# Kernel optimization log

Hardware: AMD Instinct MI355X
Metric: run time of the kernel (lower is better)

Reference implementation:

```python
import jax, jax.numpy as jnp
import numpy as np

# Llama config (TinyLlama-scale)
L, H, KVH, D = 2, 32, 8, 64      # layers, q heads, kv heads, head_dim
DM, FF, V = 2048, 8192, 32000    # d_model, intermediate, vocab
B, S = 1, 1024                   # batch, seq_len
EPS, THETA = 1e-5, 10000.0


def setup_inputs() -> dict:
    key = jax.random.key(0)
    ks = jax.random.split(key, 10)
    w = lambda k, shape: jax.random.normal(k, shape, jnp.float32) * 0.02
    return {
        "input_ids": jax.random.randint(ks[0], (B, S), 0, V, dtype=jnp.int32),
        "embed": w(ks[1], (V, DM)),
        "wq": w(ks[2], (L, DM, H * D)),
        "wk": w(ks[3], (L, DM, KVH * D)),
        "wv": w(ks[4], (L, DM, KVH * D)),
        "wo": w(ks[5], (L, H * D, DM)),
        "wgate": w(ks[6], (L, DM, FF)),
        "wup": w(ks[7], (L, DM, FF)),
        "wdown": w(ks[8], (L, FF, DM)),
        "ln1": jnp.ones((L, DM), jnp.float32),
        "ln2": jnp.ones((L, DM), jnp.float32),
    }


def _rms(h, g):
    return h * jax.lax.rsqrt(jnp.mean(h * h, axis=-1, keepdims=True) + EPS) * g


def _rotate_half(t):
    t1, t2 = jnp.split(t, 2, axis=-1)
    return jnp.concatenate([-t2, t1], axis=-1)


def reference(input_ids, embed, wq, wk, wv, wo, wgate, wup, wdown, ln1, ln2):
    x = embed[input_ids]                                  # (B,S,DM)
    # rotary embeddings (HF llama style)
    inv_freq = 1.0 / (THETA ** (jnp.arange(0, D, 2, dtype=jnp.float32) / D))
    freqs = jnp.arange(S, dtype=jnp.float32)[:, None] * inv_freq[None, :]
    emb = jnp.concatenate([freqs, freqs], axis=-1)        # (S,D)
    cos = jnp.cos(emb)[None, None]                        # (1,1,S,D)
    sin = jnp.sin(emb)[None, None]
    # eager causal additive mask (1,1,S,S)
    mask = jnp.triu(jnp.full((1, 1, S, S), jnp.finfo(jnp.float32).min, jnp.float32), k=1)
    scale = 1.0 / np.sqrt(D).astype(np.float32)
    for l in range(L):
        # self-attention block
        h = _rms(x, ln1[l])
        q = (h @ wq[l]).reshape(B, S, H, D).transpose(0, 2, 1, 3)     # (B,H,S,D)
        k = (h @ wk[l]).reshape(B, S, KVH, D).transpose(0, 2, 1, 3)   # (B,KVH,S,D)
        v = (h @ wv[l]).reshape(B, S, KVH, D).transpose(0, 2, 1, 3)
        q = q * cos + _rotate_half(q) * sin
        k = k * cos + _rotate_half(k) * sin
        k = jnp.repeat(k, H // KVH, axis=1)                           # GQA expand
        v = jnp.repeat(v, H // KVH, axis=1)
        scores = jnp.einsum('bhqd,bhkd->bhqk', q, k) * scale + mask   # eager path
        probs = jax.nn.softmax(scores, axis=-1)
        attn = jnp.einsum('bhqk,bhkd->bhqd', probs, v)
        attn = attn.transpose(0, 2, 1, 3).reshape(B, S, H * D)
        x = x + attn @ wo[l]
        # SwiGLU MLP block
        h = _rms(x, ln2[l])
        x = x + (jax.nn.silu(h @ wgate[l]) * (h @ wup[l])) @ wdown[l]
    return x
```

## Files before the change

kernel.cpp:

```cpp
#include <hip/hip_runtime.h>
#include <hip/hip_bf16.h>
#include <math.h>

#define NL 2
#define NH 32
#define NKVH 8
#define HD 64
#define DM 2048
#define FF 8192
#define SEQ 1024
#define QKVW 3072
#define RMS_EPS 1e-5f

typedef short s8v __attribute__((ext_vector_type(8)));
typedef short s4v __attribute__((ext_vector_type(4)));
typedef float f32x4 __attribute__((ext_vector_type(4)));
typedef __hip_bfloat16 bf16;

__global__ __launch_bounds__(256) void embed_kernel(const int* __restrict__ ids,
                                                    const float* __restrict__ emb,
                                                    float* __restrict__ x) {
    int s = blockIdx.x;
    int row = ids[s];
    const float4* src = (const float4*)(emb + (size_t)row * DM);
    float4* dst = (float4*)(x + (size_t)s * DM);
    #pragma unroll
    for (int i = 0; i < 2; ++i)
        dst[threadIdx.x + i * 256] = src[threadIdx.x + i * 256];
}

__global__ __launch_bounds__(256) void rms_kernel(const float* __restrict__ x,
                                                  const float* __restrict__ g,
                                                  bf16* __restrict__ out) {
    int s = blockIdx.x;
    const float4* row = (const float4*)(x + (size_t)s * DM);
    float4 v0 = row[threadIdx.x * 2];
    float4 v1 = row[threadIdx.x * 2 + 1];
    float ss = v0.x*v0.x + v0.y*v0.y + v0.z*v0.z + v0.w*v0.w
             + v1.x*v1.x + v1.y*v1.y + v1.z*v1.z + v1.w*v1.w;
    #pragma unroll
    for (int o = 32; o > 0; o >>= 1) ss += __shfl_down(ss, o, 64);
    __shared__ float red[4];
    if ((threadIdx.x & 63) == 0) red[threadIdx.x >> 6] = ss;
    __syncthreads();
    float total = red[0] + red[1] + red[2] + red[3];
    float inv = 1.0f / sqrtf(total / (float)DM + RMS_EPS);
    const float4* g4 = (const float4*)g;
    float4 ga = g4[threadIdx.x * 2], gb = g4[threadIdx.x * 2 + 1];
    union { bf16 h[8]; s8v v; } u;
    u.h[0] = __float2bfloat16(v0.x * inv * ga.x);
    u.h[1] = __float2bfloat16(v0.y * inv * ga.y);
    u.h[2] = __float2bfloat16(v0.z * inv * ga.z);
    u.h[3] = __float2bfloat16(v0.w * inv * ga.w);
    u.h[4] = __float2bfloat16(v1.x * inv * gb.x);
    u.h[5] = __float2bfloat16(v1.y * inv * gb.y);
    u.h[6] = __float2bfloat16(v1.z * inv * gb.z);
    u.h[7] = __float2bfloat16(v1.w * inv * gb.w);
    *(s8v*)(out + (size_t)s * DM + threadIdx.x * 8) = u.v;
}

template<bool OUTBF>
__global__ __launch_bounds__(256) void gemm_f32w_kernel(const bf16* __restrict__ A, int Ka,
                                                        const float* __restrict__ Wa, int Na,
                                                        const float* __restrict__ Wb, int Nb,
                                                        const float* __restrict__ Wc,
                                                        float* __restrict__ C,
                                                        bf16* __restrict__ Cb,
                                                        int M, int N, int Kchunk) {
    __shared__ bf16 As[2][128 * 64];
    __shared__ bf16 Bs[2][128 * 64];
    const int t = threadIdx.x, lane = t & 63;
    const int w = t >> 6;
    const int m0 = blockIdx.y * 128, n0 = blockIdx.x * 128;
    const size_t koff = (size_t)blockIdx.z * Kchunk;

    const int nl = t & 127;
    const int kob = t >> 7;
    const int ng = n0 + nl;
    const float* wp; int wstr;
    if (ng < Na)           { wp = Wa + ng;             wstr = Na; }
    else if (ng < Na + Nb) { wp = Wb + (ng - Na);      wstr = Nb; }
    else                   { wp = Wc + (ng - Na - Nb); wstr = N - Na - Nb; }
    wp += koff * (size_t)wstr;

    const int ako = t & 7, am = t >> 3;
    const bf16* apt = A + (size_t)(m0 + am) * Ka + koff + ako * 8;

    const int wm = (w >> 1) * 64, wn = (w & 1) * 64;
    const int fr = lane & 15, sl = lane >> 4;

    f32x4 acc[4][4];
    f32x4 z = {0.f, 0.f, 0.f, 0.f};
    #pragma unroll
    for (int i = 0; i < 4; ++i)
        #pragma unroll
        for (int j = 0; j < 4; ++j) acc[i][j] = z;

    float rb[4][8];
    s8v ra[4];

    auto LOADR = [&](int tile) {
        const int k0 = tile * 64;
        #pragma unroll
        for (int u = 0; u < 4; ++u) {
            const float* p = wp + (size_t)(k0 + (kob + 2 * u) * 8) * wstr;
            #pragma unroll
            for (int j = 0; j < 8; ++j) rb[u][j] = p[(size_t)j * wstr];
            ra[u] = *(const s8v*)(apt + (size_t)(32 * u) * Ka + k0);
        }
    };
    auto WRITE = [&](bf16* AsB, bf16* BsB) {
        #pragma unroll
        for (int u = 0; u < 4; ++u) {
            union { bf16 h[8]; s8v v; } cv;
            #pragma unroll
            for (int j = 0; j < 8; ++j) cv.h[j] = __float2bfloat16(rb[u][j]);
            int ko = kob + 2 * u;
            *(s8v*)((char*)BsB + nl * 128 + ((ko * 16) ^ ((nl & 7) << 4))) = cv.v;
            int m = am + 32 * u;
            *(s8v*)((char*)AsB + m * 128 + ((ako * 16) ^ ((m & 7) << 4))) = ra[u];
        }
    };
    auto COMPUTE = [&](const bf16* AsB, const bf16* BsB) {
        #pragma unroll
        for (int kk = 0; kk < 2; ++kk) {
            const int kb = kk * 64 + sl * 16;
            s8v af[4], bfv[4];
            #pragma unroll
            for (int i = 0; i < 4; ++i) {
                int m = wm + i * 16 + fr;
                af[i] = *(const s8v*)((const char*)AsB + m * 128 + (kb ^ ((m & 7) << 4)));
            }
            #pragma unroll
            for (int j = 0; j < 4; ++j) {
                int n = wn + j * 16 + fr;
                bfv[j] = *(const s8v*)((const char*)BsB + n * 128 + (kb ^ ((n & 7) << 4)));
            }
            #pragma unroll
            for (int i = 0; i < 4; ++i)
                #pragma unroll
                for (int j = 0; j < 4; ++j)
                    acc[i][j] = __builtin_amdgcn_mfma_f32_16x16x32_bf16(af[i], bfv[j], acc[i][j], 0, 0, 0);
        }
    };

    const int nt = Kchunk / 64;
    LOADR(0);
    WRITE(&As[0][0], &Bs[0][0]);
    __syncthreads();
    for (int tt = 0; tt < nt; ++tt) {
        const int cur = tt & 1;
        if (tt + 1 < nt) LOADR(tt + 1);
        COMPUTE(&As[cur][0], &Bs[cur][0]);
        if (tt + 1 < nt) {
            __syncthreads();
            WRITE(&As[cur ^ 1][0], &Bs[cur ^ 1][0]);
            __syncthreads();
        }
    }

    float* Cz = C + (size_t)blockIdx.z * M * N;
    #pragma unroll
    for (int i = 0; i < 4; ++i) {
        #pragma unroll
        for (int j = 0; j < 4; ++j) {
            #pragma unroll
            for (int q = 0; q < 4; ++q) {
                int row = m0 + wm + i * 16 + sl * 4 + q;
                int col = n0 + wn + j * 16 + fr;
                float vv = acc[i][j][q];
                if constexpr (OUTBF) Cb[(size_t)row * N + col] = __float2bfloat16(vv);
                else                 Cz[(size_t)row * N + col] = vv;
            }
        }
    }
}

__global__ __launch_bounds__(256) void reduce4_kernel(float* __restrict__ x,
                                                      const float* __restrict__ p) {
    const int n4 = SEQ * DM / 4;
    int i = blockIdx.x * 256 + threadIdx.x;
    if (i >= n4) return;
    float4 a = ((const float4*)x)[i];
    #pragma unroll
    for (int c = 0; c < 4; ++c) {
        float4 v = ((const float4*)p)[i + c * n4];
        a.x += v.x; a.y += v.y; a.z += v.z; a.w += v.w;
    }
    ((float4*)x)[i] = a;
}

__global__ __launch_bounds__(256) void rope_qk_kernel(const float* __restrict__ qkv,
                                                      bf16* __restrict__ Qh,
                                                      bf16* __restrict__ Kh) {
    int idx = blockIdx.x * 256 + threadIdx.x;
    int i = idx & 31;
    int hh = (idx >> 5) % (NH + NKVH);
    int s = idx / (32 * (NH + NKVH));
    bool isq = hh < NH;
    int col = isq ? hh * HD + i : DM + (hh - NH) * HD + i;
    float a = qkv[(size_t)s * QKVW + col];
    float b = qkv[(size_t)s * QKVW + col + 32];
    float inv = exp2f(-(float)i * 0.41524101186092029f);
    float ang = (float)s * inv;
    float c = cosf(ang), sn = sinf(ang);
    float ra = a * c - b * sn;
    float rb = b * c + a * sn;
    if (isq) {
        bf16* p = Qh + ((size_t)hh * SEQ + s) * HD + i;
        p[0]  = __float2bfloat16(ra);
        p[32] = __float2bfloat16(rb);
    } else {
        bf16* p = Kh + ((size_t)(hh - NH) * SEQ + s) * HD + i;
        p[0]  = __float2bfloat16(ra);
        p[32] = __float2bfloat16(rb);
    }
}

__global__ __launch_bounds__(256) void vtrans_kernel(const float* __restrict__ qkv,
                                                     bf16* __restrict__ Vt) {
    __shared__ float tile[64][65];
    const int s0 = blockIdx.x * 64;
    const int kvh = blockIdx.y;
    const int tx = threadIdx.x & 63, ty = threadIdx.x >> 6;
    #pragma unroll
    for (int i = 0; i < 16; ++i)
        tile[i * 4 + ty][tx] = qkv[(size_t)(s0 + i * 4 + ty) * QKVW + DM + 512 + kvh * HD + tx];
    __syncthreads();
    #pragma unroll
    for (int i = 0; i < 16; ++i) {
        int d = i * 4 + ty;
        Vt[((size_t)kvh * HD + d) * SEQ + s0 + tx] = __float2bfloat16(tile[tx][d]);
    }
}

__global__ __launch_bounds__(256) void attn_mfma_kernel(const bf16* __restrict__ Qh,
                                                        const bf16* __restrict__ Kh,
                                                        const bf16* __restrict__ Vt,
                                                        bf16* __restrict__ o) {
    __shared__ char lds[32768];
    char* Qs = lds;
    char* Ks = lds + 8192;
    char* Vs = lds + 16384;
    char* Ps = lds + 24576;
    const int t = threadIdx.x, lane = t & 63, w = t >> 6;
    const int g = lane >> 4, lo = lane & 15;
    const int h = blockIdx.y, kvh = h >> 2;
    const int qbase = blockIdx.x * 64;
    const int strip = w * 16;
    const bf16* qsrc = Qh + ((size_t)h * SEQ + qbase) * HD;
    const bf16* ksrc = Kh + (size_t)kvh * SEQ * HD;
    const bf16* vsrc = Vt + (size_t)kvh * HD * SEQ;

    #pragma unroll
    for (int c = t; c < 512; c += 256) {
        int row = c >> 3, col = c & 7;
        *(s8v*)(Qs + row * 128 + ((col * 16) ^ ((row & 7) << 4))) =
            *(const s8v*)(qsrc + row * HD + col * 8);
    }

    f32x4 oacc[4];
    f32x4 z = {0.f, 0.f, 0.f, 0.f};
    #pragma unroll
    for (int dj = 0; dj < 4; ++dj) oacc[dj] = z;
    float m0[4], lsum[4];
    #pragma unroll
    for (int r = 0; r < 4; ++r) { m0[r] = -INFINITY; lsum[r] = 0.f; }

    const int qt = blockIdx.x;
    for (int kt = 0; kt <= qt; ++kt) {
        __syncthreads();
        const bf16* kq = ksrc + (size_t)(kt * 64) * HD;
        const bf16* vq = vsrc + kt * 64;
        #pragma unroll
        for (int c = t; c < 512; c += 256) {
            int row = c >> 3, col = c & 7;
            int swz = (col * 16) ^ ((row & 7) << 4);
            *(s8v*)(Ks + row * 128 + swz) = *(const s8v*)(kq + row * HD + col * 8);
            *(s8v*)(Vs + row * 128 + swz) = *(const s8v*)(vq + (size_t)row * SEQ + col * 8);
        }
        __syncthreads();

        s8v qa0 = *(const s8v*)(Qs + (strip + lo) * 128 + ((g * 16) ^ ((lo & 7) << 4)));
        s8v qa1 = *(const s8v*)(Qs + (strip + lo) * 128 + ((64 + g * 16) ^ ((lo & 7) << 4)));
        f32x4 sacc[4];
        #pragma unroll
        for (int j = 0; j < 4; ++j) {
            s8v kb0 = *(const s8v*)(Ks + (j * 16 + lo) * 128 + ((g * 16) ^ ((lo & 7) << 4)));
            s8v kb1 = *(const s8v*)(Ks + (j * 16 + lo) * 128 + ((64 + g * 16) ^ ((lo & 7) << 4)));
            f32x4 sv = __builtin_amdgcn_mfma_f32_16x16x32_bf16(qa0, kb0, z, 0, 0, 0);
            sacc[j] = __builtin_amdgcn_mfma_f32_16x16x32_bf16(qa1, kb1, sv, 0, 0, 0);
        }
        #pragma unroll
        for (int j = 0; j < 4; ++j) {
            int kgl = kt * 64 + j * 16 + lo;
            #pragma unroll
            for (int r = 0; r < 4; ++r) {
                int qgl = qbase + strip + g * 4 + r;
                float sv = sacc[j][r] * 0.125f;
                sacc[j][r] = (kgl <= qgl) ? sv : -INFINITY;
            }
        }
        float rmax[4], resc[4];
        #pragma unroll
        for (int r = 0; r < 4; ++r) {
            float mx = fmaxf(fmaxf(sacc[0][r], sacc[1][r]), fmaxf(sacc[2][r], sacc[3][r]));
            mx = fmaxf(mx, __shfl_xor(mx, 1, 64));
            mx = fmaxf(mx, __shfl_xor(mx, 2, 64));
            mx = fmaxf(mx, __shfl_xor(mx, 4, 64));
            mx = fmaxf(mx, __shfl_xor(mx, 8, 64));
            float mn = fmaxf(m0[r], mx);
            resc[r] = expf(m0[r] - mn);
            m0[r] = mn;
            rmax[r] = mn;
        }
        #pragma unroll
        for (int j = 0; j < 4; ++j)
            #pragma unroll
            for (int r = 0; r < 4; ++r)
                sacc[j][r] = expf(sacc[j][r] - rmax[r]);
        #pragma unroll
        for (int r = 0; r < 4; ++r) {
            float ps = sacc[0][r] + sacc[1][r] + sacc[2][r] + sacc[3][r];
            lsum[r] = lsum[r] * resc[r] + ps;
        }
        #pragma unroll
        for (int dj = 0; dj < 4; ++dj)
            #pragma unroll
            for (int r = 0; r < 4; ++r)
                oacc[dj][r] *= resc[r];
        #pragma unroll
        for (int j = 0; j < 4; ++j) {
            #pragma unroll
            for (int r = 0; r < 4; ++r) {
                int prow = strip + g * 4 + r;
                int pcol = j * 16 + lo;
                *(bf16*)(Ps + prow * 128 + ((pcol * 2) ^ ((prow & 7) << 4))) =
                    __float2bfloat16(sacc[j][r]);
            }
        }
        s8v pa0 = *(const s8v*)(Ps + (strip + lo) * 128 + ((g * 16) ^ ((lo & 7) << 4)));
        s8v pa1 = *(const s8v*)(Ps + (strip + lo) * 128 + ((64 + g * 16) ^ ((lo & 7) << 4)));
        #pragma unroll
        for (int dj = 0; dj < 4; ++dj) {
            s8v vb0 = *(const s8v*)(Vs + (dj * 16 + lo) * 128 + ((g * 16) ^ ((lo & 7) << 4)));
            s8v vb1 = *(const s8v*)(Vs + (dj * 16 + lo) * 128 + ((64 + g * 16) ^ ((lo & 7) << 4)));
            oacc[dj] = __builtin_amdgcn_mfma_f32_16x16x32_bf16(pa0, vb0, oacc[dj], 0, 0, 0);
            oacc[dj] = __builtin_amdgcn_mfma_f32_16x16x32_bf16(pa1, vb1, oacc[dj], 0, 0, 0);
        }
    }
    float invl[4];
    #pragma unroll
    for (int r = 0; r < 4; ++r) {
        float l = lsum[r];
        l += __shfl_xor(l, 1, 64);
        l += __shfl_xor(l, 2, 64);
        l += __shfl_xor(l, 4, 64);
        l += __shfl_xor(l, 8, 64);
        invl[r] = 1.f / l;
    }
    #pragma unroll
    for (int dj = 0; dj < 4; ++dj) {
        #pragma unroll
        for (int r = 0; r < 4; ++r) {
            int qrow = qbase + strip + g * 4 + r;
            o[(size_t)qrow * DM + h * HD + dj * 16 + lo] =
                __float2bfloat16(oacc[dj][r] * invl[r]);
        }
    }
}

__global__ __launch_bounds__(256) void silu_mul_kernel(const bf16* __restrict__ gu,
                                                       bf16* __restrict__ ga) {
    int i = blockIdx.x * 256 + threadIdx.x;
    int s = i >> 10;
    int c8 = i & 1023;
    union { s8v v; bf16 h[8]; } gv, uv, ov;
    gv.v = *(const s8v*)(gu + (size_t)s * (2 * FF) + c8 * 8);
    uv.v = *(const s8v*)(gu + (size_t)s * (2 * FF) + FF + c8 * 8);
    #pragma unroll
    for (int j = 0; j < 8; ++j) {
        float g = __bfloat162float(gv.h[j]);
        float u = __bfloat162float(uv.h[j]);
        ov.h[j] = __float2bfloat16(g / (1.f + expf(-g)) * u);
    }
    *(s8v*)(ga + (size_t)s * FF + c8 * 8) = ov.v;
}

extern "C" void kernel_launch(void* const* d_in, const int* in_sizes, int n_in,
                              void* d_out, int out_size, void* d_ws, size_t ws_size,
                              hipStream_t stream) {
    const int*   ids   = (const int*)d_in[0];
    const float* emb   = (const float*)d_in[1];
    const float* wq    = (const float*)d_in[2];
    const float* wk    = (const float*)d_in[3];
    const float* wv    = (const float*)d_in[4];
    const float* wo    = (const float*)d_in[5];
    const float* wgate = (const float*)d_in[6];
    const float* wup   = (const float*)d_in[7];
    const float* wdown = (const float*)d_in[8];
    const float* ln1   = (const float*)d_in[9];
    const float* ln2   = (const float*)d_in[10];
    float* x = (float*)d_out;

    bf16* h_bf  = (bf16*)d_ws;
    bf16* attnb = h_bf  + (size_t)SEQ * DM;
    bf16* gub   = attnb + (size_t)SEQ * DM;
    bf16* gab   = gub   + (size_t)SEQ * 2 * FF;
    bf16* Qhb   = gab   + (size_t)SEQ * FF;
    bf16* Khb   = Qhb   + (size_t)NH * SEQ * HD;
    bf16* Vtb   = Khb   + (size_t)NKVH * SEQ * HD;
    float* qkv  = (float*)(Vtb + (size_t)NKVH * HD * SEQ);
    float* psum = qkv + (size_t)SEQ * QKVW;

    embed_kernel<<<SEQ, 256, 0, stream>>>(ids, emb, x);

    for (int l = 0; l < NL; ++l) {
        const float* wq_l = wq + (size_t)l * DM * DM;
        const float* wk_l = wk + (size_t)l * DM * 512;
        const float* wv_l = wv + (size_t)l * DM * 512;
        const float* wo_l = wo + (size_t)l * DM * DM;
        const float* wg_l = wgate + (size_t)l * DM * FF;
        const float* wu_l = wup   + (size_t)l * DM * FF;
        const float* wd_l = wdown + (size_t)l * FF * DM;

        rms_kernel<<<SEQ, 256, 0, stream>>>(x, ln1 + (size_t)l * DM, h_bf);

        gemm_f32w_kernel<false><<<dim3(QKVW / 128, SEQ / 128, 1), 256, 0, stream>>>(
            h_bf, DM, wq_l, DM, wk_l, 512, wv_l, qkv, nullptr, SEQ, QKVW, DM);

        rope_qk_kernel<<<(SEQ * (NH + NKVH) * 32) / 256, 256, 0, stream>>>(qkv, Qhb, Khb);
        vtrans_kernel<<<dim3(SEQ / 64, NKVH), 256, 0, stream>>>(qkv, Vtb);

        attn_mfma_kernel<<<dim3(SEQ / 64, NH), 256, 0, stream>>>(Qhb, Khb, Vtb, attnb);

        gemm_f32w_kernel<false><<<dim3(DM / 128, SEQ / 128, 4), 256, 0, stream>>>(
            attnb, DM, wo_l, DM, nullptr, 0, nullptr, psum, nullptr, SEQ, DM, DM / 4);
        reduce4_kernel<<<(SEQ * DM / 4) / 256, 256, 0, stream>>>(x, psum);

        rms_kernel<<<SEQ, 256, 0, stream>>>(x, ln2 + (size_t)l * DM, h_bf);

        gemm_f32w_kernel<true><<<dim3((2 * FF) / 128, SEQ / 128, 1), 256, 0, stream>>>(
            h_bf, DM, wg_l, FF, wu_l, FF, nullptr, nullptr, gub, SEQ, 2 * FF, DM);

        silu_mul_kernel<<<(SEQ * FF / 8) / 256, 256, 0, stream>>>(gub, gab);

        gemm_f32w_kernel<false><<<dim3(DM / 128, SEQ / 128, 4), 256, 0, stream>>>(
            gab, FF, wd_l, DM, nullptr, 0, nullptr, psum, nullptr, SEQ, DM, FF / 4);
        reduce4_kernel<<<(SEQ * DM / 4) / 256, 256, 0, stream>>>(x, psum);
    }
}
```

Measured before the change: 648.7 us.

## Remap GEMM blocks per XCD, shrink K tile, split-K the QKV projection

The GEMM kernel now decodes a 1-D block index so blocks sharing the same N columns of weights land on the same XCD, which should improve L2 reuse of the fp32 weight reads. The K tile drops from 64 to 32 with a padded 80-byte LDS row and a new swizzle, cutting LDS to 40 KB so that launch_bounds(256,3) can keep more blocks resident. The QKV projection becomes split-K by 2, followed by a generalized reduction kernel. The trade-offs are more loop iterations and barriers per block, plus an extra reduction pass for QKV.

```diff
diff --git a/kernel.cpp b/kernel.cpp
--- a/kernel.cpp
+++ b/kernel.cpp
@@ -60,22 +60,24 @@
 }
 
 template<bool OUTBF>
-__global__ __launch_bounds__(256) void gemm_f32w_kernel(const bf16* __restrict__ A, int Ka,
-                                                        const float* __restrict__ Wa, int Na,
-                                                        const float* __restrict__ Wb, int Nb,
-                                                        const float* __restrict__ Wc,
-                                                        float* __restrict__ C,
-                                                        bf16* __restrict__ Cb,
-                                                        int M, int N, int Kchunk) {
-    __shared__ bf16 As[2][128 * 64];
-    __shared__ bf16 Bs[2][128 * 64];
-    const int t = threadIdx.x, lane = t & 63;
-    const int w = t >> 6;
-    const int m0 = blockIdx.y * 128, n0 = blockIdx.x * 128;
+__global__ __launch_bounds__(256, 3) void gemm_f32w_kernel(const bf16* __restrict__ A, int Ka,
+                                                           const float* __restrict__ Wa, int Na,
+                                                           const float* __restrict__ Wb, int Nb,
+                                                           const float* __restrict__ Wc,
+                                                           float* __restrict__ C,
+                                                           bf16* __restrict__ Cb,
+                                                           int M, int N, int Kchunk,
+                                                           int nPerXcd) {
+    __shared__ char lds[40960];
+    const int t = threadIdx.x, lane = t & 63, w = t >> 6;
+    const int orig = blockIdx.x;
+    const int xcd = orig & 7, local = orig >> 3;
+    const int m_b = local & 7;
+    const int n_b = xcd * nPerXcd + (local >> 3);
+    const int m0 = m_b * 128, n0 = n_b * 128;
     const size_t koff = (size_t)blockIdx.z * Kchunk;
 
-    const int nl = t & 127;
-    const int kob = t >> 7;
+    const int nl = t & 127, kh = t >> 7;
     const int ng = n0 + nl;
     const float* wp; int wstr;
     if (ng < Na)           { wp = Wa + ng;             wstr = Na; }
@@ -83,8 +85,8 @@
     else                   { wp = Wc + (ng - Na - Nb); wstr = N - Na - Nb; }
     wp += koff * (size_t)wstr;
 
-    const int ako = t & 7, am = t >> 3;
-    const bf16* apt = A + (size_t)(m0 + am) * Ka + koff + ako * 8;
+    const int am = t >> 1, ah = t & 1;
+    const bf16* apt = A + (size_t)(m0 + am) * Ka + koff + ah * 16;
 
     const int wm = (w >> 1) * 64, wn = (w & 1) * 64;
     const int fr = lane & 15, sl = lane >> 4;
@@ -96,65 +98,60 @@
         #pragma unroll
         for (int j = 0; j < 4; ++j) acc[i][j] = z;
 
-    float rb[4][8];
-    s8v ra[4];
+    float rbv[16];
+    s8v ra0, ra1;
 
     auto LOADR = [&](int tile) {
-        const int k0 = tile * 64;
-        #pragma unroll
-        for (int u = 0; u < 4; ++u) {
-            const float* p = wp + (size_t)(k0 + (kob + 2 * u) * 8) * wstr;
-            #pragma unroll
-            for (int j = 0; j < 8; ++j) rb[u][j] = p[(size_t)j * wstr];
-            ra[u] = *(const s8v*)(apt + (size_t)(32 * u) * Ka + k0);
-        }
+        const int k0 = tile * 32;
+        const float* p = wp + (size_t)(k0 + kh * 16) * wstr;
+        #pragma unroll
+        for (int j = 0; j < 16; ++j) rbv[j] = p[(size_t)j * wstr];
+        ra0 = *(const s8v*)(apt + k0);
+        ra1 = *(const s8v*)(apt + k0 + 8);
     };
-    auto WRITE = [&](bf16* AsB, bf16* BsB) {
-        #pragma unroll
-        for (int u = 0; u < 4; ++u) {
-            union { bf16 h[8]; s8v v; } cv;
-            #pragma unroll
-            for (int j = 0; j < 8; ++j) cv.h[j] = __float2bfloat16(rb[u][j]);
-            int ko = kob + 2 * u;
-            *(s8v*)((char*)BsB + nl * 128 + ((ko * 16) ^ ((nl & 7) << 4))) = cv.v;
-            int m = am + 32 * u;
-            *(s8v*)((char*)AsB + m * 128 + ((ako * 16) ^ ((m & 7) << 4))) = ra[u];
-        }
+    auto WRITE = [&](int buf) {
+        char* aw = lds + buf * 10240 + am * 80 + ((ah * 32) ^ (((am >> 3) & 1) << 5));
+        *(s8v*)aw = ra0;
+        *(s8v*)(aw + 16) = ra1;
+        union { bf16 h[16]; s8v v[2]; } cv;
+        #pragma unroll
+        for (int j = 0; j < 16; ++j) cv.h[j] = __float2bfloat16(rbv[j]);
+        char* bw = lds + 20480 + buf * 10240 + nl * 80 + ((kh * 32) ^ (((nl >> 3) & 1) << 5));
+        *(s8v*)bw = cv.v[0];
+        *(s8v*)(bw + 16) = cv.v[1];
     };
-    auto COMPUTE = [&](const bf16* AsB, const bf16* BsB) {
-        #pragma unroll
-        for (int kk = 0; kk < 2; ++kk) {
-            const int kb = kk * 64 + sl * 16;
-            s8v af[4], bfv[4];
-            #pragma unroll
-            for (int i = 0; i < 4; ++i) {
-                int m = wm + i * 16 + fr;
-                af[i] = *(const s8v*)((const char*)AsB + m * 128 + (kb ^ ((m & 7) << 4)));
-            }
-            #pragma unroll
-            for (int j = 0; j < 4; ++j) {
-                int n = wn + j * 16 + fr;
-                bfv[j] = *(const s8v*)((const char*)BsB + n * 128 + (kb ^ ((n & 7) << 4)));
-            }
-            #pragma unroll
-            for (int i = 0; i < 4; ++i)
-                #pragma unroll
-                for (int j = 0; j < 4; ++j)
-                    acc[i][j] = __builtin_amdgcn_mfma_f32_16x16x32_bf16(af[i], bfv[j], acc[i][j], 0, 0, 0);
-        }
+    auto COMPUTE = [&](int buf) {
+        const char* Ab = lds + buf * 10240;
+        const char* Bb = lds + 20480 + buf * 10240;
+        s8v af[4], bfv[4];
+        #pragma unroll
+        for (int i = 0; i < 4; ++i) {
+            int m = wm + i * 16 + fr;
+            af[i] = *(const s8v*)(Ab + m * 80 + ((sl * 16) ^ (((m >> 3) & 1) << 5)));
+        }
+        #pragma unroll
+        for (int j = 0; j < 4; ++j) {
+            int n = wn + j * 16 + fr;
+            bfv[j] = *(const s8v*)(Bb + n * 80 + ((sl * 16) ^ (((n >> 3) & 1) << 5)));
+        }
+        #pragma unroll
+        for (int i = 0; i < 4; ++i)
+            #pragma unroll
+            for (int j = 0; j < 4; ++j)
+                acc[i][j] = __builtin_amdgcn_mfma_f32_16x16x32_bf16(af[i], bfv[j], acc[i][j], 0, 0, 0);
     };
 
-    const int nt = Kchunk / 64;
+    const int nt = Kchunk / 32;
     LOADR(0);
-    WRITE(&As[0][0], &Bs[0][0]);
+    WRITE(0);
     __syncthreads();
     for (int tt = 0; tt < nt; ++tt) {
         const int cur = tt & 1;
         if (tt + 1 < nt) LOADR(tt + 1);
-        COMPUTE(&As[cur][0], &Bs[cur][0]);
+        COMPUTE(cur);
         if (tt + 1 < nt) {
             __syncthreads();
-            WRITE(&As[cur ^ 1][0], &Bs[cur ^ 1][0]);
+            WRITE(cur ^ 1);
             __syncthreads();
         }
     }
@@ -176,18 +173,20 @@
     }
 }
 
-__global__ __launch_bounds__(256) void reduce4_kernel(float* __restrict__ x,
-                                                      const float* __restrict__ p) {
-    const int n4 = SEQ * DM / 4;
+__global__ __launch_bounds__(256) void reduceN_kernel(float* __restrict__ dst,
+                                                      const float* __restrict__ p,
+                                                      int n4, int slices, int addto,
+                                                      size_t stride4) {
     int i = blockIdx.x * 256 + threadIdx.x;
     if (i >= n4) return;
-    float4 a = ((const float4*)x)[i];
-    #pragma unroll
-    for (int c = 0; c < 4; ++c) {
-        float4 v = ((const float4*)p)[i + c * n4];
+    float4 a;
+    if (addto) a = ((const float4*)dst)[i];
+    else { a.x = a.y = a.z = a.w = 0.f; }
+    for (int c = 0; c < slices; ++c) {
+        float4 v = ((const float4*)p)[i + c * stride4];
         a.x += v.x; a.y += v.y; a.z += v.z; a.w += v.w;
     }
-    ((float4*)x)[i] = a;
+    ((float4*)dst)[i] = a;
 }
 
 __global__ __launch_bounds__(256) void rope_qk_kernel(const float* __restrict__ qkv,
@@ -426,27 +425,31 @@
 
         rms_kernel<<<SEQ, 256, 0, stream>>>(x, ln1 + (size_t)l * DM, h_bf);
 
-        gemm_f32w_kernel<false><<<dim3(QKVW / 128, SEQ / 128, 1), 256, 0, stream>>>(
-            h_bf, DM, wq_l, DM, wk_l, 512, wv_l, qkv, nullptr, SEQ, QKVW, DM);
+        gemm_f32w_kernel<false><<<dim3(24 * 8, 1, 2), 256, 0, stream>>>(
+            h_bf, DM, wq_l, DM, wk_l, 512, wv_l, psum, nullptr, SEQ, QKVW, DM / 2, 3);
+        reduceN_kernel<<<(SEQ * QKVW / 4 + 255) / 256, 256, 0, stream>>>(
+            qkv, psum, SEQ * QKVW / 4, 2, 0, (size_t)SEQ * QKVW / 4);
 
         rope_qk_kernel<<<(SEQ * (NH + NKVH) * 32) / 256, 256, 0, stream>>>(qkv, Qhb, Khb);
         vtrans_kernel<<<dim3(SEQ / 64, NKVH), 256, 0, stream>>>(qkv, Vtb);
 
         attn_mfma_kernel<<<dim3(SEQ / 64, NH), 256, 0, stream>>>(Qhb, Khb, Vtb, attnb);
 
-        gemm_f32w_kernel<false><<<dim3(DM / 128, SEQ / 128, 4), 256, 0, stream>>>(
-            attnb, DM, wo_l, DM, nullptr, 0, nullptr, psum, nullptr, SEQ, DM, DM / 4);
-        reduce4_kernel<<<(SEQ * DM / 4) / 256, 256, 0, stream>>>(x, psum);
+        gemm_f32w_kernel<false><<<dim3(16 * 8, 1, 4), 256, 0, stream>>>(
+            attnb, DM, wo_l, DM, nullptr, 0, nullptr, psum, nullptr, SEQ, DM, DM / 4, 2);
+        reduceN_kernel<<<(SEQ * DM / 4 + 255) / 256, 256, 0, stream>>>(
+            x, psum, SEQ * DM / 4, 4, 1, (size_t)SEQ * DM / 4);
 
         rms_kernel<<<SEQ, 256, 0, stream>>>(x, ln2 + (size_t)l * DM, h_bf);
 
-        gemm_f32w_kernel<true><<<dim3((2 * FF) / 128, SEQ / 128, 1), 256, 0, stream>>>(
-            h_bf, DM, wg_l, FF, wu_l, FF, nullptr, nullptr, gub, SEQ, 2 * FF, DM);
+        gemm_f32w_kernel<true><<<dim3(128 * 8, 1, 1), 256, 0, stream>>>(
+            h_bf, DM, wg_l, FF, wu_l, FF, nullptr, nullptr, gub, SEQ, 2 * FF, DM, 16);
 
         silu_mul_kernel<<<(SEQ * FF / 8) / 256, 256, 0, stream>>>(gub, gab);
 
-        gemm_f32w_kernel<false><<<dim3(DM / 128, SEQ / 128, 4), 256, 0, stream>>>(
-            gab, FF, wd_l, DM, nullptr, 0, nullptr, psum, nullptr, SEQ, DM, FF / 4);
-        reduce4_kernel<<<(SEQ * DM / 4) / 256, 256, 0, stream>>>(x, psum);
-    }
-}
+        gemm_f32w_kernel<false><<<dim3(16 * 8, 1, 4), 256, 0, stream>>>(
+            gab, FF, wd_l, DM, nullptr, 0, nullptr, psum, nullptr, SEQ, DM, FF / 4, 2);
+        reduceN_kernel<<<(SEQ * DM / 4 + 255) / 256, 256, 0, stream>>>(
+            x, psum, SEQ * DM / 4, 4, 1, (size_t)SEQ * DM / 4);
+    }
+}
```

New measurement: 761.6 us. +17.4%, slower.
